# Optimization experiments

Hardware: AMD Instinct MI355X
Metric: run time of the kernel (lower is better)

## Reference

```python
import jax, jax.numpy as jnp
import numpy as np

B, T, F, H, O = 4096, 200, 64, 16, 1

def setup_inputs() -> dict:
    key = jax.random.key(0)
    ks = jax.random.split(key, 7)
    s = 1.0 / np.sqrt(H)
    return {
        "input_samples": jax.random.normal(ks[0], (B, T, F), dtype=jnp.float32),
        # LSTM params, PyTorch gate order (i, f, g, o)
        "W_ih": jax.random.uniform(ks[1], (4 * H, F), jnp.float32, -s, s),
        "W_hh": jax.random.uniform(ks[2], (4 * H, H), jnp.float32, -s, s),
        "b_ih": jax.random.uniform(ks[3], (4 * H,), jnp.float32, -s, s),
        "b_hh": jax.random.uniform(ks[4], (4 * H,), jnp.float32, -s, s),
        # final Linear(H -> O)
        "W_out": jax.random.uniform(ks[5], (O, H), jnp.float32, -s, s),
        "b_out": jax.random.uniform(ks[6], (O,), jnp.float32, -s, s),
    }

def reference(input_samples, W_ih, W_hh, b_ih, b_hh, W_out, b_out):
    x = input_samples  # [B, T, F]
    h = W_hh.shape[1]
    # precompute input contribution to gates for all timesteps: [B, T, 4H]
    gx = jnp.einsum('btf,gf->btg', x, W_ih) + b_ih + b_hh

    def step(carry, gx_t):
        h_t, c_t = carry
        g = gx_t + h_t @ W_hh.T  # [B, 4H]
        i, f, gg, o = jnp.split(g, 4, axis=-1)
        i = jax.nn.sigmoid(i)
        f = jax.nn.sigmoid(f)
        gg = jnp.tanh(gg)
        o = jax.nn.sigmoid(o)
        c_new = f * c_t + i * gg
        h_new = o * jnp.tanh(c_new)
        return (h_new, c_new), None

    h0 = jnp.zeros((x.shape[0], h), x.dtype)
    (hT, _cT), _ = jax.lax.scan(step, (h0, h0), jnp.swapaxes(gx, 0, 1))
    # squeeze(h_n) -> [B, H]; Linear + sigmoid -> [B, O]
    return jax.nn.sigmoid(hT @ W_out.T + b_out)
```

## Files before the change

### kernel.cpp

```cpp
#include <hip/hip_runtime.h>


#define Bsz 4096
#define Tn  200
#define Fn  64
#define Hn  16
#define CS  8
#define NCH 25

#define CM1 -1.4426950408889634f
#define CM2 -2.8853900817779268f

typedef _Float16 half8 __attribute__((ext_vector_type(8)));
typedef _Float16 half4 __attribute__((ext_vector_type(4)));
typedef float    f32x4 __attribute__((ext_vector_type(4)));

__device__ __forceinline__ half8 to_half8(const float4& a, const float4& b) {
    half8 h;
    h[0] = (_Float16)a.x; h[1] = (_Float16)a.y; h[2] = (_Float16)a.z; h[3] = (_Float16)a.w;
    h[4] = (_Float16)b.x; h[5] = (_Float16)b.y; h[6] = (_Float16)b.z; h[7] = (_Float16)b.w;
    return h;
}

__device__ __forceinline__ float sigm(float z) {
    return __builtin_amdgcn_rcpf(1.0f + __builtin_amdgcn_exp2f(z * CM1));
}
__device__ __forceinline__ float tanhe(float z) {
    return fmaf(2.0f, __builtin_amdgcn_rcpf(
        1.0f + __builtin_amdgcn_exp2f(z * CM2)), -1.0f);
}
__device__ __forceinline__ float tanhp(float x) {
    float u   = x * x;
    float num = x * fmaf(u, u + 105.0f, 945.0f);
    float den = fmaf(u, fmaf(15.0f, u, 420.0f), 945.0f);
    float th  = num * __builtin_amdgcn_rcpf(den);
    return fminf(fmaxf(th, -1.0f), 1.0f);
}

__device__ __forceinline__ void lds_barrier() {
    __builtin_amdgcn_sched_barrier(0);
    asm volatile("s_waitcnt lgkmcnt(0)" ::: "memory");
    __builtin_amdgcn_s_barrier();
    __builtin_amdgcn_sched_barrier(0);
}

__global__ __launch_bounds__(192, 1) void lstm_fused(
    const float* __restrict__ x,
    const float* __restrict__ Wih,
    const float* __restrict__ Whh,
    const float* __restrict__ bih,
    const float* __restrict__ bhh,
    const float* __restrict__ Wout,
    const float* __restrict__ bout,
    float* __restrict__ out)
{
    const int lane = threadIdx.x & 63;
    const int wave = threadIdx.x >> 6;
    const int l15  = lane & 15;
    const int lhi  = lane >> 4;
    const int b    = (int)blockIdx.x * 16 + l15;

    __shared__ f32x4 gxbuf[3][CS][4][64];

    half8 WihF[4][2];
    f32x4 biasC[4];
    float4 xr[4][4];
    const int pofs = (wave - 1) * 4;
    const float* xl = x + (size_t)b * (Tn * Fn) + lhi * 8;

    if (wave >= 1) {
#pragma unroll
        for (int m = 0; m < 4; ++m)
#pragma unroll
            for (int kh = 0; kh < 2; ++kh) {
                const float* wr = Wih + (m * 16 + l15) * Fn + kh * 32 + lhi * 8;
                float4 w0 = *reinterpret_cast<const float4*>(wr);
                float4 w1 = *reinterpret_cast<const float4*>(wr + 4);
                WihF[m][kh] = to_half8(w0, w1);
            }
#pragma unroll
        for (int m = 0; m < 4; ++m) {
            float4 v0 = *reinterpret_cast<const float4*>(bih + m * 16 + lhi * 4);
            float4 v1 = *reinterpret_cast<const float4*>(bhh + m * 16 + lhi * 4);
            biasC[m][0] = v0.x + v1.x; biasC[m][1] = v0.y + v1.y;
            biasC[m][2] = v0.z + v1.z; biasC[m][3] = v0.w + v1.w;
        }
#pragma unroll
        for (int s = 0; s < 4; ++s) {
            const float* xp = xl + (pofs + s) * Fn;
            xr[s][0] = *reinterpret_cast<const float4*>(xp);
            xr[s][1] = *reinterpret_cast<const float4*>(xp + 4);
            xr[s][2] = *reinterpret_cast<const float4*>(xp + 32);
            xr[s][3] = *reinterpret_cast<const float4*>(xp + 36);
        }
    }

    half4 WhhF[4];
#pragma unroll
    for (int m = 0; m < 4; ++m) {
        float4 w = *reinterpret_cast<const float4*>(Whh + (m * 16 + l15) * Hn + lhi * 4);
        WhhF[m][0] = (_Float16)w.x; WhhF[m][1] = (_Float16)w.y;
        WhhF[m][2] = (_Float16)w.z; WhhF[m][3] = (_Float16)w.w;
    }

    f32x4 cst = { 0.0f, 0.0f, 0.0f, 0.0f };
    half4 hHi = { 0, 0, 0, 0 };
    float hcur[4] = { 0.0f, 0.0f, 0.0f, 0.0f };

    auto recur = [&](f32x4 (&g)[4]) {
        f32x4 pre1 = __builtin_amdgcn_mfma_f32_16x16x16f16(WhhF[1], hHi, g[1], 0, 0, 0);
        f32x4 pre0 = __builtin_amdgcn_mfma_f32_16x16x16f16(WhhF[0], hHi, g[0], 0, 0, 0);
        f32x4 pre2 = __builtin_amdgcn_mfma_f32_16x16x16f16(WhhF[2], hHi, g[2], 0, 0, 0);
        f32x4 pre3 = __builtin_amdgcn_mfma_f32_16x16x16f16(WhhF[3], hHi, g[3], 0, 0, 0);
#pragma unroll
        for (int r = 0; r < 4; ++r) {
            float fg = sigm(pre1[r]);
            float ig = sigm(pre0[r]);
            float gg = tanhe(pre2[r]);
            float og = sigm(pre3[r]);
            cst[r]  = fmaf(fg, cst[r], ig * gg);
            hcur[r] = og * tanhp(cst[r]);
        }
        auto p01 = __builtin_amdgcn_cvt_pkrtz(hcur[0], hcur[1]);
        auto p23 = __builtin_amdgcn_cvt_pkrtz(hcur[2], hcur[3]);
        hHi[0] = (_Float16)p01[0]; hHi[1] = (_Float16)p01[1];
        hHi[2] = (_Float16)p23[0]; hHi[3] = (_Float16)p23[1];
    };

#pragma unroll 1
    for (int i = 0; i < NCH + 2; ++i) {
        lds_barrier();
        if (wave >= 1) {
            if (i < NCH) {
                const int bi  = i % 3;
                const int cnx = (i + 1 < NCH) ? i + 1 : NCH - 1;
#pragma unroll
                for (int s = 0; s < 4; ++s) {
                    half8 f0 = to_half8(xr[s][0], xr[s][1]);
                    half8 f1 = to_half8(xr[s][2], xr[s][3]);
                    const float* xp = xl + (size_t)(cnx * CS + pofs + s) * Fn;
                    xr[s][0] = *reinterpret_cast<const float4*>(xp);
                    xr[s][1] = *reinterpret_cast<const float4*>(xp + 4);
                    xr[s][2] = *reinterpret_cast<const float4*>(xp + 32);
                    xr[s][3] = *reinterpret_cast<const float4*>(xp + 36);
#pragma unroll
                    for (int m = 0; m < 4; ++m) {
                        f32x4 acc = __builtin_amdgcn_mfma_f32_16x16x32_f16(
                            WihF[m][0], f0, biasC[m], 0, 0, 0);
                        acc = __builtin_amdgcn_mfma_f32_16x16x32_f16(
                            WihF[m][1], f1, acc, 0, 0, 0);
                        gxbuf[bi][pofs + s][m][lane] = acc;
                    }
                }
            }
        } else {
            if (i >= 2) {
                const int bi = (i - 2) % 3;
                f32x4 gA[4], gB[4];
#pragma unroll
                for (int m = 0; m < 4; ++m) gA[m] = gxbuf[bi][0][m][lane];
#pragma unroll
                for (int m = 0; m < 4; ++m) gB[m] = gxbuf[bi][1][m][lane];
                recur(gA);
#pragma unroll
                for (int m = 0; m < 4; ++m) gA[m] = gxbuf[bi][2][m][lane];
                recur(gB);
#pragma unroll
                for (int m = 0; m < 4; ++m) gB[m] = gxbuf[bi][3][m][lane];
                recur(gA);
#pragma unroll
                for (int m = 0; m < 4; ++m) gA[m] = gxbuf[bi][4][m][lane];
                recur(gB);
#pragma unroll
                for (int m = 0; m < 4; ++m) gB[m] = gxbuf[bi][5][m][lane];
                recur(gA);
#pragma unroll
                for (int m = 0; m < 4; ++m) gA[m] = gxbuf[bi][6][m][lane];
                recur(gB);
#pragma unroll
                for (int m = 0; m < 4; ++m) gB[m] = gxbuf[bi][7][m][lane];
                recur(gA);
                recur(gB);
            }
        }
    }

    if (wave == 0) {
        float4 wo = *reinterpret_cast<const float4*>(Wout + lhi * 4);
        float po = hcur[0] * wo.x;
        po = fmaf(hcur[1], wo.y, po);
        po = fmaf(hcur[2], wo.z, po);
        po = fmaf(hcur[3], wo.w, po);
        po += __shfl_xor(po, 16);
        po += __shfl_xor(po, 32);
        if (lhi == 0)
            out[b] = sigm(po + bout[0]);
    }
}

extern "C" void kernel_launch(void* const* d_in, const int* in_sizes, int n_in,
                              void* d_out, int out_size, void* d_ws, size_t ws_size,
                              hipStream_t stream) {
    const float* x    = (const float*)d_in[0];
    const float* Wih  = (const float*)d_in[1];
    const float* Whh  = (const float*)d_in[2];
    const float* bih  = (const float*)d_in[3];
    const float* bhh  = (const float*)d_in[4];
    const float* Wout = (const float*)d_in[5];
    const float* bout = (const float*)d_in[6];
    float* out = (float*)d_out;

    lstm_fused<<<dim3(Bsz / 16), dim3(192), 0, stream>>>(
        x, Wih, Whh, bih, bhh, Wout, bout, out);
}
```

Measured before the change: 78.29 us.

## Replace block barriers with LDS flag-based producer/consumer handoff

Removes the per-chunk workgroup barrier that lock-stepped the two producer waves with the recurrence wave. It replaces it with LDS counters that wave 0 and the producers spin on with acquire/release atomics and s_sleep. Producers can now run up to three chunks ahead without waiting on every chunk. It also swaps the rational tanh approximation for the exp-based tanh on the cell state. Risks are spin-wait polling overhead and memory-ordering subtleties in the handoff.

```diff
diff --git a/kernel.cpp b/kernel.cpp
--- a/kernel.cpp
+++ b/kernel.cpp
@@ -28,20 +28,6 @@
 __device__ __forceinline__ float tanhe(float z) {
     return fmaf(2.0f, __builtin_amdgcn_rcpf(
         1.0f + __builtin_amdgcn_exp2f(z * CM2)), -1.0f);
-}
-__device__ __forceinline__ float tanhp(float x) {
-    float u   = x * x;
-    float num = x * fmaf(u, u + 105.0f, 945.0f);
-    float den = fmaf(u, fmaf(15.0f, u, 420.0f), 945.0f);
-    float th  = num * __builtin_amdgcn_rcpf(den);
-    return fminf(fmaxf(th, -1.0f), 1.0f);
-}
-
-__device__ __forceinline__ void lds_barrier() {
-    __builtin_amdgcn_sched_barrier(0);
-    asm volatile("s_waitcnt lgkmcnt(0)" ::: "memory");
-    __builtin_amdgcn_s_barrier();
-    __builtin_amdgcn_sched_barrier(0);
 }
 
 __global__ __launch_bounds__(192, 1) void lstm_fused(
@@ -61,6 +47,12 @@
     const int b    = (int)blockIdx.x * 16 + l15;
 
     __shared__ f32x4 gxbuf[3][CS][4][64];
+    __shared__ int prod_done[2];
+    __shared__ int cons_done;
+
+    if (threadIdx.x == 0) {
+        prod_done[0] = 0; prod_done[1] = 0; cons_done = 0;
+    }
 
     half8 WihF[4][2];
     f32x4 biasC[4];
@@ -119,7 +111,7 @@
             float gg = tanhe(pre2[r]);
             float og = sigm(pre3[r]);
             cst[r]  = fmaf(fg, cst[r], ig * gg);
-            hcur[r] = og * tanhp(cst[r]);
+            hcur[r] = og * tanhe(cst[r]);
         }
         auto p01 = __builtin_amdgcn_cvt_pkrtz(hcur[0], hcur[1]);
         auto p23 = __builtin_amdgcn_cvt_pkrtz(hcur[2], hcur[3]);
@@ -127,65 +119,80 @@
         hHi[2] = (_Float16)p23[0]; hHi[3] = (_Float16)p23[1];
     };
 
+    __syncthreads();
+
+    if (wave >= 1) {
+        const int pg = wave - 1;
 #pragma unroll 1
-    for (int i = 0; i < NCH + 2; ++i) {
-        lds_barrier();
-        if (wave >= 1) {
-            if (i < NCH) {
-                const int bi  = i % 3;
-                const int cnx = (i + 1 < NCH) ? i + 1 : NCH - 1;
-#pragma unroll
-                for (int s = 0; s < 4; ++s) {
-                    half8 f0 = to_half8(xr[s][0], xr[s][1]);
-                    half8 f1 = to_half8(xr[s][2], xr[s][3]);
-                    const float* xp = xl + (size_t)(cnx * CS + pofs + s) * Fn;
-                    xr[s][0] = *reinterpret_cast<const float4*>(xp);
-                    xr[s][1] = *reinterpret_cast<const float4*>(xp + 4);
-                    xr[s][2] = *reinterpret_cast<const float4*>(xp + 32);
-                    xr[s][3] = *reinterpret_cast<const float4*>(xp + 36);
-#pragma unroll
-                    for (int m = 0; m < 4; ++m) {
-                        f32x4 acc = __builtin_amdgcn_mfma_f32_16x16x32_f16(
-                            WihF[m][0], f0, biasC[m], 0, 0, 0);
-                        acc = __builtin_amdgcn_mfma_f32_16x16x32_f16(
-                            WihF[m][1], f1, acc, 0, 0, 0);
-                        gxbuf[bi][pofs + s][m][lane] = acc;
-                    }
+        for (int i = 0; i < NCH; ++i) {
+            if (i >= 3) {
+                while (__hip_atomic_load(&cons_done, __ATOMIC_ACQUIRE,
+                                         __HIP_MEMORY_SCOPE_WORKGROUP) < i - 2)
+                    __builtin_amdgcn_s_sleep(1);
+            }
+            const int bi  = i % 3;
+            const int cnx = (i + 1 < NCH) ? i + 1 : NCH - 1;
+#pragma unroll
+            for (int s = 0; s < 4; ++s) {
+                half8 f0 = to_half8(xr[s][0], xr[s][1]);
+                half8 f1 = to_half8(xr[s][2], xr[s][3]);
+                const float* xp = xl + (size_t)(cnx * CS + pofs + s) * Fn;
+                xr[s][0] = *reinterpret_cast<const float4*>(xp);
+                xr[s][1] = *reinterpret_cast<const float4*>(xp + 4);
+                xr[s][2] = *reinterpret_cast<const float4*>(xp + 32);
+                xr[s][3] = *reinterpret_cast<const float4*>(xp + 36);
+#pragma unroll
+                for (int m = 0; m < 4; ++m) {
+                    f32x4 acc = __builtin_amdgcn_mfma_f32_16x16x32_f16(
+                        WihF[m][0], f0, biasC[m], 0, 0, 0);
+                    acc = __builtin_amdgcn_mfma_f32_16x16x32_f16(
+                        WihF[m][1], f1, acc, 0, 0, 0);
+                    gxbuf[bi][pofs + s][m][lane] = acc;
                 }
             }
-        } else {
-            if (i >= 2) {
-                const int bi = (i - 2) % 3;
-                f32x4 gA[4], gB[4];
-#pragma unroll
-                for (int m = 0; m < 4; ++m) gA[m] = gxbuf[bi][0][m][lane];
-#pragma unroll
-                for (int m = 0; m < 4; ++m) gB[m] = gxbuf[bi][1][m][lane];
-                recur(gA);
-#pragma unroll
-                for (int m = 0; m < 4; ++m) gA[m] = gxbuf[bi][2][m][lane];
-                recur(gB);
-#pragma unroll
-                for (int m = 0; m < 4; ++m) gB[m] = gxbuf[bi][3][m][lane];
-                recur(gA);
-#pragma unroll
-                for (int m = 0; m < 4; ++m) gA[m] = gxbuf[bi][4][m][lane];
-                recur(gB);
-#pragma unroll
-                for (int m = 0; m < 4; ++m) gB[m] = gxbuf[bi][5][m][lane];
-                recur(gA);
-#pragma unroll
-                for (int m = 0; m < 4; ++m) gA[m] = gxbuf[bi][6][m][lane];
-                recur(gB);
-#pragma unroll
-                for (int m = 0; m < 4; ++m) gB[m] = gxbuf[bi][7][m][lane];
-                recur(gA);
-                recur(gB);
-            }
-        }
-    }
-
-    if (wave == 0) {
+            if (lane == 0)
+                __hip_atomic_store(&prod_done[pg], i + 1, __ATOMIC_RELEASE,
+                                   __HIP_MEMORY_SCOPE_WORKGROUP);
+        }
+    } else {
+#pragma unroll 1
+        for (int j = 0; j < NCH; ++j) {
+            while (__hip_atomic_load(&prod_done[0], __ATOMIC_ACQUIRE,
+                                     __HIP_MEMORY_SCOPE_WORKGROUP) < j + 1 ||
+                   __hip_atomic_load(&prod_done[1], __ATOMIC_ACQUIRE,
+                                     __HIP_MEMORY_SCOPE_WORKGROUP) < j + 1)
+                __builtin_amdgcn_s_sleep(1);
+            const int bi = j % 3;
+            f32x4 gA[4], gB[4];
+#pragma unroll
+            for (int m = 0; m < 4; ++m) gA[m] = gxbuf[bi][0][m][lane];
+#pragma unroll
+            for (int m = 0; m < 4; ++m) gB[m] = gxbuf[bi][1][m][lane];
+            recur(gA);
+#pragma unroll
+            for (int m = 0; m < 4; ++m) gA[m] = gxbuf[bi][2][m][lane];
+            recur(gB);
+#pragma unroll
+            for (int m = 0; m < 4; ++m) gB[m] = gxbuf[bi][3][m][lane];
+            recur(gA);
+#pragma unroll
+            for (int m = 0; m < 4; ++m) gA[m] = gxbuf[bi][4][m][lane];
+            recur(gB);
+#pragma unroll
+            for (int m = 0; m < 4; ++m) gB[m] = gxbuf[bi][5][m][lane];
+            recur(gA);
+#pragma unroll
+            for (int m = 0; m < 4; ++m) gA[m] = gxbuf[bi][6][m][lane];
+            recur(gB);
+#pragma unroll
+            for (int m = 0; m < 4; ++m) gB[m] = gxbuf[bi][7][m][lane];
+            recur(gA);
+            recur(gB);
+            if (lane == 0)
+                __hip_atomic_store(&cons_done, j + 1, __ATOMIC_RELEASE,
+                                   __HIP_MEMORY_SCOPE_WORKGROUP);
+        }
+
         float4 wo = *reinterpret_cast<const float4*>(Wout + lhi * 4);
         float po = hcur[0] * wo.x;
         po = fmaf(hcur[1], wo.y, po);
```

After: 73.99 us. -5.5%, faster.

## Fold exp2 scale into LSTM weights and share reciprocals across gate pairs

Applied to the files above, without the earlier changes.

Pre-multiplies W_ih, W_hh and the combined bias by -log2(e) (or -2log2(e) for the g gate), so the recurrent MFMA outputs feed exp2 directly without a scale multiply. The gate algebra is rewritten: i*g becomes (1-eg)/((1+ei)(1+eg)) and o*tanh(c) becomes (1-ec)/((1+eo)(1+ec)). Pairs of reciprocals are computed with a single rcp (1/(ab) times b and a), which cuts transcendental instructions on the serial recurrence critical path. In exchange it adds multiplies, risks overflow or inf in the products when exponents are large, and the fp16 weights carry extra scaling error.

```diff
diff --git a/kernel.cpp b/kernel.cpp
--- a/kernel.cpp
+++ b/kernel.cpp
@@ -15,26 +15,23 @@
 typedef _Float16 half4 __attribute__((ext_vector_type(4)));
 typedef float    f32x4 __attribute__((ext_vector_type(4)));
 
-__device__ __forceinline__ half8 to_half8(const float4& a, const float4& b) {
+__device__ __forceinline__ half8 to_half8s(const float4& a, const float4& b, float s) {
     half8 h;
-    h[0] = (_Float16)a.x; h[1] = (_Float16)a.y; h[2] = (_Float16)a.z; h[3] = (_Float16)a.w;
-    h[4] = (_Float16)b.x; h[5] = (_Float16)b.y; h[6] = (_Float16)b.z; h[7] = (_Float16)b.w;
+    h[0] = (_Float16)(a.x * s); h[1] = (_Float16)(a.y * s);
+    h[2] = (_Float16)(a.z * s); h[3] = (_Float16)(a.w * s);
+    h[4] = (_Float16)(b.x * s); h[5] = (_Float16)(b.y * s);
+    h[6] = (_Float16)(b.z * s); h[7] = (_Float16)(b.w * s);
     return h;
 }
 
 __device__ __forceinline__ float sigm(float z) {
     return __builtin_amdgcn_rcpf(1.0f + __builtin_amdgcn_exp2f(z * CM1));
 }
-__device__ __forceinline__ float tanhe(float z) {
-    return fmaf(2.0f, __builtin_amdgcn_rcpf(
-        1.0f + __builtin_amdgcn_exp2f(z * CM2)), -1.0f);
-}
-__device__ __forceinline__ float tanhp(float x) {
-    float u   = x * x;
-    float num = x * fmaf(u, u + 105.0f, 945.0f);
-    float den = fmaf(u, fmaf(15.0f, u, 420.0f), 945.0f);
-    float th  = num * __builtin_amdgcn_rcpf(den);
-    return fminf(fmaxf(th, -1.0f), 1.0f);
+
+__device__ __forceinline__ void pair_rcp(float a, float b, float& ra, float& rb) {
+    float rp = __builtin_amdgcn_rcpf(a * b);
+    ra = rp * b;
+    rb = rp * a;
 }
 
 __device__ __forceinline__ void lds_barrier() {
@@ -62,6 +59,8 @@
 
     __shared__ f32x4 gxbuf[3][CS][4][64];
 
+    const float scm[4] = { CM1, CM1, CM2, CM1 };
+
     half8 WihF[4][2];
     f32x4 biasC[4];
     float4 xr[4][4];
@@ -70,20 +69,19 @@
 
     if (wave >= 1) {
 #pragma unroll
-        for (int m = 0; m < 4; ++m)
+        for (int m = 0; m < 4; ++m) {
+            const float s = scm[m];
 #pragma unroll
             for (int kh = 0; kh < 2; ++kh) {
                 const float* wr = Wih + (m * 16 + l15) * Fn + kh * 32 + lhi * 8;
                 float4 w0 = *reinterpret_cast<const float4*>(wr);
                 float4 w1 = *reinterpret_cast<const float4*>(wr + 4);
-                WihF[m][kh] = to_half8(w0, w1);
+                WihF[m][kh] = to_half8s(w0, w1, s);
             }
-#pragma unroll
-        for (int m = 0; m < 4; ++m) {
             float4 v0 = *reinterpret_cast<const float4*>(bih + m * 16 + lhi * 4);
             float4 v1 = *reinterpret_cast<const float4*>(bhh + m * 16 + lhi * 4);
-            biasC[m][0] = v0.x + v1.x; biasC[m][1] = v0.y + v1.y;
-            biasC[m][2] = v0.z + v1.z; biasC[m][3] = v0.w + v1.w;
+            biasC[m][0] = (v0.x + v1.x) * s; biasC[m][1] = (v0.y + v1.y) * s;
+            biasC[m][2] = (v0.z + v1.z) * s; biasC[m][3] = (v0.w + v1.w) * s;
         }
 #pragma unroll
         for (int s = 0; s < 4; ++s) {
@@ -98,9 +96,10 @@
     half4 WhhF[4];
 #pragma unroll
     for (int m = 0; m < 4; ++m) {
+        const float s = scm[m];
         float4 w = *reinterpret_cast<const float4*>(Whh + (m * 16 + l15) * Hn + lhi * 4);
-        WhhF[m][0] = (_Float16)w.x; WhhF[m][1] = (_Float16)w.y;
-        WhhF[m][2] = (_Float16)w.z; WhhF[m][3] = (_Float16)w.w;
+        WhhF[m][0] = (_Float16)(w.x * s); WhhF[m][1] = (_Float16)(w.y * s);
+        WhhF[m][2] = (_Float16)(w.z * s); WhhF[m][3] = (_Float16)(w.w * s);
     }
 
     f32x4 cst = { 0.0f, 0.0f, 0.0f, 0.0f };
@@ -108,19 +107,41 @@
     float hcur[4] = { 0.0f, 0.0f, 0.0f, 0.0f };
 
     auto recur = [&](f32x4 (&g)[4]) {
-        f32x4 pre1 = __builtin_amdgcn_mfma_f32_16x16x16f16(WhhF[1], hHi, g[1], 0, 0, 0);
-        f32x4 pre0 = __builtin_amdgcn_mfma_f32_16x16x16f16(WhhF[0], hHi, g[0], 0, 0, 0);
-        f32x4 pre2 = __builtin_amdgcn_mfma_f32_16x16x16f16(WhhF[2], hHi, g[2], 0, 0, 0);
-        f32x4 pre3 = __builtin_amdgcn_mfma_f32_16x16x16f16(WhhF[3], hHi, g[3], 0, 0, 0);
+        f32x4 pf = __builtin_amdgcn_mfma_f32_16x16x16f16(WhhF[1], hHi, g[1], 0, 0, 0);
+        f32x4 pi = __builtin_amdgcn_mfma_f32_16x16x16f16(WhhF[0], hHi, g[0], 0, 0, 0);
+        f32x4 pg = __builtin_amdgcn_mfma_f32_16x16x16f16(WhhF[2], hHi, g[2], 0, 0, 0);
+        f32x4 po = __builtin_amdgcn_mfma_f32_16x16x16f16(WhhF[3], hHi, g[3], 0, 0, 0);
+
+        float df[4], dig[4], eg[4], eo[4];
 #pragma unroll
         for (int r = 0; r < 4; ++r) {
-            float fg = sigm(pre1[r]);
-            float ig = sigm(pre0[r]);
-            float gg = tanhe(pre2[r]);
-            float og = sigm(pre3[r]);
-            cst[r]  = fmaf(fg, cst[r], ig * gg);
-            hcur[r] = og * tanhp(cst[r]);
-        }
+            float ef = __builtin_amdgcn_exp2f(pf[r]);
+            float ei = __builtin_amdgcn_exp2f(pi[r]);
+            eg[r]    = __builtin_amdgcn_exp2f(pg[r]);
+            eo[r]    = __builtin_amdgcn_exp2f(po[r]);
+            df[r]  = 1.0f + ef;
+            dig[r] = (1.0f + ei) * (1.0f + eg[r]);
+        }
+        float rf[4], rig[4];
+        pair_rcp(df[0],  df[1],  rf[0],  rf[1]);
+        pair_rcp(df[2],  df[3],  rf[2],  rf[3]);
+        pair_rcp(dig[0], dig[1], rig[0], rig[1]);
+        pair_rcp(dig[2], dig[3], rig[2], rig[3]);
+
+        float ec[4], dh[4];
+#pragma unroll
+        for (int r = 0; r < 4; ++r) {
+            cst[r] = fmaf(rf[r], cst[r], (1.0f - eg[r]) * rig[r]);
+            ec[r]  = __builtin_amdgcn_exp2f(cst[r] * CM2);
+            dh[r]  = (1.0f + eo[r]) * (1.0f + ec[r]);
+        }
+        float rh[4];
+        pair_rcp(dh[0], dh[1], rh[0], rh[1]);
+        pair_rcp(dh[2], dh[3], rh[2], rh[3]);
+#pragma unroll
+        for (int r = 0; r < 4; ++r)
+            hcur[r] = (1.0f - ec[r]) * rh[r];
+
         auto p01 = __builtin_amdgcn_cvt_pkrtz(hcur[0], hcur[1]);
         auto p23 = __builtin_amdgcn_cvt_pkrtz(hcur[2], hcur[3]);
         hHi[0] = (_Float16)p01[0]; hHi[1] = (_Float16)p01[1];
@@ -136,8 +157,8 @@
                 const int cnx = (i + 1 < NCH) ? i + 1 : NCH - 1;
 #pragma unroll
                 for (int s = 0; s < 4; ++s) {
-                    half8 f0 = to_half8(xr[s][0], xr[s][1]);
-                    half8 f1 = to_half8(xr[s][2], xr[s][3]);
+                    half8 f0 = to_half8s(xr[s][0], xr[s][1], 1.0f);
+                    half8 f1 = to_half8s(xr[s][2], xr[s][3], 1.0f);
                     const float* xp = xl + (size_t)(cnx * CS + pofs + s) * Fn;
                     xr[s][0] = *reinterpret_cast<const float4*>(xp);
                     xr[s][1] = *reinterpret_cast<const float4*>(xp + 4);
```

New measurement: 66.20 us. 1.18x faster.
